# Kernel tuning notes

Hardware: AMD Instinct MI355X
Metric: run time of the kernel (lower is better)

The kernel has to match this reference:

```python
import jax, jax.numpy as jnp
import numpy as np

N_NODES, NUM_FEAT, EMB, HID, N_CLASSES, N_EDGES = 800, 111, 32, 200, 15, 8000
ALPHA = 0.5   # DirGNNConv default mixing
EPS = 1e-5    # LayerNorm eps


def _pade_coeffs(deg=5):
    # [5/5] Pade approximant of sqrt(1 - x) (as in FastDifferentiableMatSqrt)
    K = 2 * deg + 1
    b = np.zeros(K); b[0] = 1.0
    for k in range(1, K):
        b[k] = b[k - 1] * (0.5 - (k - 1)) / k
    c = b * ((-1.0) ** np.arange(K))  # Taylor coeffs of sqrt(1-x)
    A = np.empty((deg, deg))
    for i in range(deg):
        for j in range(1, deg + 1):
            A[i, j - 1] = c[deg + 1 + i - j]
    q = np.concatenate([[1.0], np.linalg.solve(A, -c[deg + 1:])])
    p = np.array([sum(q[j] * c[k - j] for j in range(min(k, deg) + 1)) for k in range(deg + 1)])
    return p.astype(np.float32), q.astype(np.float32)

PADE_P, PADE_Q = _pade_coeffs()


def _mpa_impl(A):
    # matrix square root via Pade approximant (MPA forward)
    normA = jnp.sqrt(jnp.sum(A * A))
    I = jnp.eye(A.shape[0], dtype=A.dtype)
    p_app = I - A / normA
    p_hat = p_app
    p_sqrt = PADE_P[0] * I
    q_sqrt = PADE_Q[0] * I
    for i in range(5):
        p_sqrt = p_sqrt + PADE_P[i + 1] * p_hat
        q_sqrt = q_sqrt + PADE_Q[i + 1] * p_hat
        p_hat = p_hat @ p_app
    return jnp.linalg.solve(q_sqrt, p_sqrt) * jnp.sqrt(normA)


@jax.custom_vjp
def mpa_lya(A):
    return _mpa_impl(A)


def _mpa_fwd(A):
    S = _mpa_impl(A)
    return S, (S, jnp.sqrt(jnp.sum(A * A)))


def _mpa_bwd(res, g):
    # iterative Lyapunov solver backward (8 coupled Newton-Schulz iterations)
    S, normA = res
    I = jnp.eye(S.shape[0], dtype=S.dtype)
    b = S / jnp.sqrt(normA)
    c = g / jnp.sqrt(normA)
    for _ in range(8):
        b2 = b @ b
        c = 0.5 * (c @ (3.0 * I - b2) - b2 @ c + b @ (c @ b))
        b = 0.5 * (b @ (3.0 * I - b2))
    return (0.5 * c,)

mpa_lya.defvjp(_mpa_fwd, _mpa_bwd)


def gcn_sparse(m, ei, n):
    # GCNConv(normalize=False): out[dst] = sum_{(src,dst) in E} (x @ W)[src]
    return jax.ops.segment_sum(m[ei[0]], ei[1], num_segments=n)


def hetero_layer_sparse(h, eis, W, b):
    # W: [3(in,out,root), 4 edge types, Fin, Fout]; HeteroConv aggr='sum'
    n = h.shape[0]
    out = jnp.zeros((n, W.shape[-1]), h.dtype)
    for e, ei in enumerate(eis):
        x_in = gcn_sparse(h @ W[0, e], ei, n) + b[0, e]
        x_out = gcn_sparse(h @ W[1, e], ei[::-1], n) + b[1, e]  # flipped edges
        out = out + ALPHA * x_out + (1.0 - ALPHA) * x_in + h @ W[2, e] + b[2, e]
    return out


def hetero_layer_dense(h, masks, W, b):
    # masks: [4, N, N] binary adjacency (src, dst); dense equivalent of scatter
    out = jnp.zeros((h.shape[0], W.shape[-1]), h.dtype)
    for e in range(masks.shape[0]):
        x_in = masks[e].T @ (h @ W[0, e]) + b[0, e]
        x_out = masks[e] @ (h @ W[1, e]) + b[1, e]
        out = out + ALPHA * x_out + (1.0 - ALPHA) * x_in + h @ W[2, e] + b[2, e]
    return out


def graph_layernorm(h, wb):
    # PyG LayerNorm mode='graph', single graph: normalize over all nodes+feats
    mu = jnp.mean(h)
    var = jnp.mean((h - mu) ** 2)
    return (h - mu) / jnp.sqrt(var + EPS) * wb[0] + wb[1]


def hetero_gnn(h, layer_fn, graph, W1, b1, W2, b2, ln):
    h = graph_layernorm(layer_fn(h, graph, W1, b1), ln[0])
    return graph_layernorm(layer_fn(h, graph, W2, b2), ln[1])


def pairwise_S(z, lin_W, lin_b, iu, ju):
    n = z.shape[0]
    M = (z[iu] - z[ju]) ** 2                        # [N(N+1)/2, HID]
    mg = jax.nn.sigmoid(M @ lin_W + lin_b)[:, 0]    # upper-tri entries, row-major
    tri = jnp.zeros((n, n), z.dtype).at[iu, ju].set(mg)
    return mpa_lya(tri)


def model_forward(x_note, embed_W, embed_b, g1_l1_W, g1_l1_b, g1_l2_W, g1_l2_b, g1_ln,
                  g2_l1_W, g2_l1_b, g2_l2_W, g2_l2_b, g2_ln, lin_W, lin_b, clf_W, clf_b,
                  eis, batch):
    n = x_note.shape[0]
    iu, ju = np.triu_indices(n)
    h = x_note @ embed_W + embed_b                   # [N, 32]
    z0 = hetero_gnn(h, hetero_layer_sparse, eis, g1_l1_W, g1_l1_b, g1_l2_W, g1_l2_b, g1_ln)
    S1 = pairwise_S(z0, lin_W, lin_b, iu, ju)
    A0 = jnp.stack([jnp.zeros((n, n), h.dtype).at[ei[0], ei[1]].set(1.0) for ei in eis])
    h = S1 @ h
    # adj_to_coord(nonzero) only keeps the binary pattern of S1 @ A @ S1
    mask1 = jnp.stack([((S1 @ A0[e]) @ S1 != 0).astype(h.dtype) for e in range(4)])
    z1 = hetero_gnn(h, hetero_layer_dense, mask1, g2_l1_W, g2_l1_b, g2_l2_W, g2_l2_b, g2_ln)
    S2 = pairwise_S(z1, lin_W, lin_b, iu, ju)
    h = S2 @ h
    mask2 = jnp.stack([((S2 @ mask1[e]) @ S2 != 0).astype(h.dtype) for e in range(4)])
    z2 = hetero_gnn(h, hetero_layer_dense, mask2, g2_l1_W, g2_l1_b, g2_l2_W, g2_l2_b, g2_ln)
    counts = jax.ops.segment_sum(jnp.ones((n,), z2.dtype), batch, num_segments=1)
    x2 = jax.ops.segment_sum(z2, batch, num_segments=1) / counts[:, None]  # global_mean_pool
    logits = x2 @ clf_W + clf_b
    return x2, jax.nn.log_softmax(logits, axis=-1), S1, S2


def setup_inputs() -> dict:
    key = jax.random.key(0)
    ks = jax.random.split(key, 14)
    N, F, E, H, NC, NE = N_NODES, NUM_FEAT, EMB, HID, N_CLASSES, N_EDGES
    def w(k, shape, fan_in):
        return (jax.random.normal(k, shape, jnp.float32) / np.sqrt(fan_in)).astype(jnp.float32)
    ln = jnp.broadcast_to(jnp.stack([jnp.ones(H, jnp.float32), jnp.zeros(H, jnp.float32)]), (2, 2, H)) + 0.0
    return dict(
        x_note=jax.random.normal(ks[0], (N, F), jnp.float32),
        embed_W=w(ks[1], (F, E), F), embed_b=jnp.zeros((E,), jnp.float32),
        g1_l1_W=w(ks[2], (3, 4, E, H), E), g1_l1_b=jnp.zeros((3, 4, H), jnp.float32),
        g1_l2_W=w(ks[3], (3, 4, H, H), H), g1_l2_b=jnp.zeros((3, 4, H), jnp.float32),
        g1_ln=ln,
        g2_l1_W=w(ks[4], (3, 4, E, H), E), g2_l1_b=jnp.zeros((3, 4, H), jnp.float32),
        g2_l2_W=w(ks[5], (3, 4, H, H), H), g2_l2_b=jnp.zeros((3, 4, H), jnp.float32),
        g2_ln=ln,
        lin_W=w(ks[6], (H, 1), H), lin_b=jnp.zeros((1,), jnp.float32),
        clf_W=w(ks[7], (H, NC), H), clf_b=jnp.zeros((NC,), jnp.float32),
        ei_forward=jax.random.randint(ks[8], (2, NE), 0, N, jnp.int32),
        ei_onset=jax.random.randint(ks[9], (2, NE), 0, N, jnp.int32),
        ei_sustain=jax.random.randint(ks[10], (2, NE), 0, N, jnp.int32),
        ei_rest=jax.random.randint(ks[11], (2, NE), 0, N, jnp.int32),
        batch=jnp.zeros((N,), jnp.int32),
    )


def reference(x_note, embed_W, embed_b, g1_l1_W, g1_l1_b, g1_l2_W, g1_l2_b, g1_ln,
              g2_l1_W, g2_l1_b, g2_l2_W, g2_l2_b, g2_ln, lin_W, lin_b, clf_W, clf_b,
              ei_forward, ei_onset, ei_sustain, ei_rest, batch):
    eis = (ei_forward, ei_onset, ei_sustain, ei_rest)
    return model_forward(x_note, embed_W, embed_b, g1_l1_W, g1_l1_b, g1_l2_W, g1_l2_b, g1_ln,
                         g2_l1_W, g2_l1_b, g2_l2_W, g2_l2_b, g2_ln, lin_W, lin_b, clf_W, clf_b,
                         eis, batch)
```

## Files before the change

### kernel.cpp

```cpp
#include <hip/hip_runtime.h>
#include <hip/hip_bf16.h>
#include <math.h>
#include <stdio.h>

static constexpr int   kN  = 800;
static constexpr int   kF  = 111;
static constexpr int   kE  = 32;
static constexpr int   kH  = 200;
static constexpr int   kNC = 15;
static constexpr int   kNE = 8000;
static constexpr long  kNN = (long)kN*kN;
static constexpr long  kNH = (long)kN*kH;
static constexpr float kAl  = 0.5f;
static constexpr float kEps = 1e-5f;
static constexpr int   kGB  = (int)((kNH+255)/256);
static constexpr int   kDB  = 50;
static constexpr int   kCH  = 50;
static constexpr int   kNCHK= kN/kCH;

typedef unsigned short u16;
typedef __attribute__((ext_vector_type(8))) short short8;
typedef __attribute__((ext_vector_type(4))) float f32x4;

__device__ __forceinline__ u16 f2bf(float v){
  __hip_bfloat16 b = __float2bfloat16(v);
  return *reinterpret_cast<u16*>(&b);
}
__device__ __forceinline__ float bf2f(u16 h){
  unsigned int u = ((unsigned int)h) << 16;
  float f; __builtin_memcpy(&f, &u, 4);
  return f;
}

enum { EPI_NONE=0, EPI_BIAS=1, EPI_SCALE=4, EPI_ACC=6, EPI_DUAL=7 };

template<bool TRANSA, bool TRIUA, bool TRIUB, int EPI, bool LNA>
__global__ __launch_bounds__(256)
void gemm_kernel(const float* __restrict__ A, int lda,
                 const float* __restrict__ B, int ldb,
                 float* __restrict__ C, int ldc,
                 int M, int Ncl, int K,
                 long sA, long sB, long sC, float scale,
                 const float* __restrict__ bias, int kstep,
                 const double* __restrict__ scalp,
                 const float* __restrict__ lnw,
                 const double* __restrict__ lnpart, int lnnb,
                 float* __restrict__ C2)
{
  constexpr int TM=64, TN=64, TK=16;
  A += (long)blockIdx.z * sA;
  B += (long)blockIdx.z * sB;
  C += (long)blockIdx.z * sC;
  __shared__ float As[TK][TM+4];
  __shared__ float Bs[TK][TN+4];
  const int tid = threadIdx.x;
  const int tn4 = (tid & 15)*4, tm4 = (tid >> 4)*4;
  const int m0 = blockIdx.x * TM, n0 = blockIdx.y * TN;
  float acc[4][4] = {};
  float mu = 0.f, rsf = 1.f;
  if (LNA){
    __shared__ double lnS[256], lnQ[256];
    double s=0.0, q=0.0;
    for (int i=tid; i<lnnb; i+=256){ s += lnpart[2*i]; q += lnpart[2*i+1]; }
    lnS[tid]=s; lnQ[tid]=q;
    __syncthreads();
    for (int h=128; h>0; h>>=1){
      if (tid < h){ lnS[tid]+=lnS[tid+h]; lnQ[tid]+=lnQ[tid+h]; }
      __syncthreads();
    }
    double m = lnS[0]/(double)kNH;
    double var = lnQ[0]/(double)kNH - m*m;
    mu = (float)m;
    rsf = rsqrtf((float)var + kEps);
    __syncthreads();
  }
  const int kbase = kstep ? (int)blockIdx.z * kstep : 0;
  int k0 = TRIUA ? max(m0 - kbase, 0) : 0;
  int kEnd = TRIUB ? min(K, n0 + TN - kbase) : K;
  const bool skip = (k0 >= kEnd);
  if (skip && EPI == EPI_ACC) return;
  if (!skip) {
    float ar[4], br[4];
    auto loadT = [&](int kk0, float* arr, float* brr){
      #pragma unroll
      for (int u=0; u<4; ++u){
        int idx = tid + 256*u;
        float av = 0.f;
        if (!TRANSA) {
          int m = idx >> 4, ka = idx & 15;
          int gm = m0+m, gk = kk0+ka;
          if (gm < M && gk < K){
            av = A[(long)gm*lda + gk];
            if (LNA) av = (av - mu)*(rsf*lnw[gk]) + lnw[kH + gk];
          }
        } else {
          int ka = idx >> 6, m = idx & 63;
          int gm = m0+m, gk = kk0+ka;
          if (gm < M && gk < K){
            av = A[(long)gk*lda + gm];
            if (LNA) av = (av - mu)*(rsf*lnw[gk]) + lnw[kH + gk];
          }
        }
        int kb = idx >> 6, nb = idx & 63;
        int gk = kk0+kb, gn = n0+nb;
        arr[u] = av;
        brr[u] = (gk < K && gn < Ncl) ? B[(long)gk*ldb + gn] : 0.f;
      }
    };
    auto storeT = [&](const float* arr, const float* brr){
      #pragma unroll
      for (int u=0; u<4; ++u){
        int idx = tid + 256*u;
        if (!TRANSA){ int m = idx>>4, ka = idx&15; As[ka][m] = arr[u]; }
        else        { int ka = idx>>6, m = idx&63; As[ka][m] = arr[u]; }
        int kb = idx>>6, nb = idx&63;
        Bs[kb][nb] = brr[u];
      }
    };
    loadT(k0, ar, br);
    for (;;){
      __syncthreads();
      storeT(ar, br);
      __syncthreads();
      int kn = k0 + TK;
      bool more = kn < kEnd;
      if (more) loadT(kn, ar, br);
      #pragma unroll
      for (int kk=0; kk<TK; ++kk) {
        float a[4], b[4];
        #pragma unroll
        for (int u=0;u<4;++u){ a[u]=As[kk][tm4+u]; b[u]=Bs[kk][tn4+u]; }
        #pragma unroll
        for (int i=0;i<4;++i)
          #pragma unroll
          for (int j=0;j<4;++j)
            acc[i][j] = fmaf(a[i], b[j], acc[i][j]);
      }
      if (!more) break;
      k0 = kn;
    }
  }
  float sc = scale;
  if ((EPI == EPI_ACC || EPI == EPI_SCALE || EPI == EPI_DUAL) && scalp)
    sc *= (float)sqrt(sqrt(scalp[0]));
  #pragma unroll
  for (int i=0;i<4;++i) {
    int gm = m0 + tm4 + i;
    if (gm >= M) continue;
    #pragma unroll
    for (int j=0;j<4;++j) {
      int gn = n0 + tn4 + j;
      if (gn >= Ncl) continue;
      float v = acc[i][j];
      long off = (long)gm*ldc + gn;
      if (EPI == EPI_BIAS)       C[off] = v + bias[gn];
      else if (EPI == EPI_SCALE) C[off] = sc*v;
      else if (EPI == EPI_ACC)   unsafeAtomicAdd(&C[off], sc*v);
      else if (EPI == EPI_DUAL){ C[off] = v; C2[off] = sc*v; }
      else                       C[off] = v;
    }
  }
}

template<bool TRANSA, bool TRIUA, bool TRIUB, int EPI, bool LNA = false>
static inline void launch_gemm(hipStream_t st,
                               const float* A, int lda, const float* B, int ldb,
                               float* C, int ldc, int M, int Ncl, int K, int batch,
                               long sA, long sB, long sC, float scale,
                               const float* bias = nullptr, int kstep = 0,
                               const double* scalp = nullptr,
                               const float* lnw = nullptr,
                               const double* lnpart = nullptr, int lnnb = 0,
                               float* C2 = nullptr)
{
  dim3 grid((M+63)/64, (Ncl+63)/64, batch);
  gemm_kernel<TRANSA,TRIUA,TRIUB,EPI,LNA><<<grid, 256, 0, st>>>(
      A,lda,B,ldb,C,ldc,M,Ncl,K,sA,sB,sC,scale,bias,kstep,scalp,lnw,lnpart,lnnb,C2);
}

__global__ __launch_bounds__(256)
void bgemm2_kernel(const u16* __restrict__ Ah, const u16* __restrict__ Al,
                   const u16* __restrict__ Bh, const u16* __restrict__ Bl,
                   float* __restrict__ C, float* __restrict__ C2,
                   u16* __restrict__ Oh, u16* __restrict__ Ol,
                   float p0, float p1)
{
  constexpr int TM=64, TN=64, BK=32;
  __shared__ u16 Ash[TM][40], Asl[TM][40], Bsh[TN][40], Bsl[TN][40];
  const int tid = threadIdx.x;
  const int m0 = blockIdx.x*TM, n0 = blockIdx.y*TN;
  const int w = tid>>6, lane = tid&63;
  const int wm = (w&1)*32, wn = (w>>1)*32;
  const int quad = lane>>4, lm = lane&15;
  f32x4 acc00={}, acc01={}, acc10={}, acc11={};
  const bool skip = (m0 > n0 + TN - 1);
  int k0 = m0;
  const int kEnd = min(kN, n0+TN);
  const int ar = tid>>2, ac = (tid&3)*8;
  if (!skip){
    uint4 avh, avl, bvh, bvl;
    auto loadT = [&](int kk0){
      avh = {0,0,0,0}; avl = {0,0,0,0}; bvh = {0,0,0,0}; bvl = {0,0,0,0};
      int gk = kk0 + ac;
      if (m0+ar < kN && gk < kN){
        avh = *(const uint4*)(Ah + (long)(m0+ar)*kN + gk);
        avl = *(const uint4*)(Al + (long)(m0+ar)*kN + gk);
      }
      if (n0+ar < kN && gk < kN){
        bvh = *(const uint4*)(Bh + (long)(n0+ar)*kN + gk);
        bvl = *(const uint4*)(Bl + (long)(n0+ar)*kN + gk);
      }
    };
    loadT(k0);
    for (;;){
      __syncthreads();
      *(uint4*)&Ash[ar][ac] = avh; *(uint4*)&Asl[ar][ac] = avl;
      *(uint4*)&Bsh[ar][ac] = bvh; *(uint4*)&Bsl[ar][ac] = bvl;
      __syncthreads();
      int kn = k0 + BK;
      bool more = kn < kEnd;
      if (more) loadT(kn);
      short8 a0h = *(const short8*)&Ash[wm+lm][quad*8];
      short8 a1h = *(const short8*)&Ash[wm+16+lm][quad*8];
      short8 a0l = *(const short8*)&Asl[wm+lm][quad*8];
      short8 a1l = *(const short8*)&Asl[wm+16+lm][quad*8];
      short8 b0h = *(const short8*)&Bsh[wn+lm][quad*8];
      short8 b1h = *(const short8*)&Bsh[wn+16+lm][quad*8];
      short8 b0l = *(const short8*)&Bsl[wn+lm][quad*8];
      short8 b1l = *(const short8*)&Bsl[wn+16+lm][quad*8];
      acc00 = __builtin_amdgcn_mfma_f32_16x16x32_bf16(a0h,b0h,acc00,0,0,0);
      acc00 = __builtin_amdgcn_mfma_f32_16x16x32_bf16(a0h,b0l,acc00,0,0,0);
      acc00 = __builtin_amdgcn_mfma_f32_16x16x32_bf16(a0l,b0h,acc00,0,0,0);
      acc01 = __builtin_amdgcn_mfma_f32_16x16x32_bf16(a0h,b1h,acc01,0,0,0);
      acc01 = __builtin_amdgcn_mfma_f32_16x16x32_bf16(a0h,b1l,acc01,0,0,0);
      acc01 = __builtin_amdgcn_mfma_f32_16x16x32_bf16(a0l,b1h,acc01,0,0,0);
      acc10 = __builtin_amdgcn_mfma_f32_16x16x32_bf16(a1h,b0h,acc10,0,0,0);
      acc10 = __builtin_amdgcn_mfma_f32_16x16x32_bf16(a1h,b0l,acc10,0,0,0);
      acc10 = __builtin_amdgcn_mfma_f32_16x16x32_bf16(a1l,b0h,acc10,0,0,0);
      acc11 = __builtin_amdgcn_mfma_f32_16x16x32_bf16(a1h,b1h,acc11,0,0,0);
      acc11 = __builtin_amdgcn_mfma_f32_16x16x32_bf16(a1h,b1l,acc11,0,0,0);
      acc11 = __builtin_amdgcn_mfma_f32_16x16x32_bf16(a1l,b1h,acc11,0,0,0);
      if (!more) break;
      k0 = kn;
    }
  }
  f32x4 accs[2][2] = {{acc00, acc01},{acc10, acc11}};
  #pragma unroll
  for (int ti=0; ti<2; ++ti){
    #pragma unroll
    for (int tj=0; tj<2; ++tj){
      #pragma unroll
      for (int r=0; r<4; ++r){
        int gm = m0 + wm + ti*16 + quad*4 + r;
        int gn = n0 + wn + tj*16 + lm;
        if (gm >= kN || gn >= kN) continue;
        float v = accs[ti][tj][r];
        long off = (long)gm*kN + gn;
        C[off]  += p0*v;
        C2[off] += p1*v;
        if (Oh){
          u16 h = f2bf(v);
          Oh[off] = h;
          Ol[off] = f2bf(v - bf2f(h));
        }
      }
    }
  }
}

__global__ __launch_bounds__(256)
void ln_pair_prep_kernel(const float* __restrict__ tnh, const double* __restrict__ part,
                         int nb, const float* __restrict__ ln, const float* __restrict__ linW,
                         u16* __restrict__ zwh, u16* __restrict__ zwl,
                         u16* __restrict__ zzh, u16* __restrict__ zzl,
                         float* __restrict__ avec, double* __restrict__ frobz)
{
  __shared__ double ss[256], qq[256];
  __shared__ float ared[256];
  const int n = blockIdx.x, t = threadIdx.x;
  if (t == 0) *frobz = 0.0;
  double s=0.0, q=0.0;
  for (int i=t; i<nb; i+=256){ s += part[2*i]; q += part[2*i+1]; }
  ss[t]=s; qq[t]=q;
  __syncthreads();
  for (int h=128; h>0; h>>=1){
    if (t < h){ ss[t]+=ss[t+h]; qq[t]+=qq[t+h]; }
    __syncthreads();
  }
  double m = ss[0]/(double)kNH;
  const float mu = (float)m;
  const float rs = rsqrtf((float)(qq[0]/(double)kNH - m*m) + kEps);
  float acc = 0.f;
  if (t < kH){
    float z = (tnh[(long)n*kH + t] - mu)*(rs*ln[t]) + ln[kH + t];
    float wv = linW[t];
    float zw = wv*z;
    long off = (long)n*kH + t;
    u16 h1 = f2bf(zw);
    zwh[off] = h1; zwl[off] = f2bf(zw - bf2f(h1));
    u16 h2 = f2bf(z);
    zzh[off] = h2; zzl[off] = f2bf(z - bf2f(h2));
    acc = zw*z;
  }
  ared[t] = acc;
  __syncthreads();
  for (int h=128; h>0; h>>=1){
    if (t < h) ared[t] += ared[t+h];
    __syncthreads();
  }
  if (t == 0) avec[n] = ared[0];
}

__global__ __launch_bounds__(256)
void bgemm_pair_kernel(const u16* __restrict__ Ah, const u16* __restrict__ Al,
                       const u16* __restrict__ Bh, const u16* __restrict__ Bl,
                       const float* __restrict__ avec, const float* __restrict__ linb,
                       float* __restrict__ tri, double* __restrict__ frob2)
{
  constexpr int TM=64, TN=64, BK=32, KK=kH;
  __shared__ u16 Ash[TM][40], Asl[TM][40], Bsh[TN][40], Bsl[TN][40];
  __shared__ float red[256];
  const int tid = threadIdx.x;
  const int m0 = blockIdx.x*TM, n0 = blockIdx.y*TN;
  if (m0 > n0 + TN - 1){
    for (int idx = tid; idx < TM*TN; idx += 256){
      int r = idx >> 6, c = idx & 63;
      int gm = m0 + r, gn = n0 + c;
      if (gm < kN && gn < kN) tri[(long)gm*kN + gn] = 0.f;
    }
    return;
  }
  const int w = tid>>6, lane = tid&63;
  const int wm = (w&1)*32, wn = (w>>1)*32;
  const int quad = lane>>4, lm = lane&15;
  f32x4 acc00={}, acc01={}, acc10={}, acc11={};
  const int ar = tid>>2, ac = (tid&3)*8;
  for (int k0 = 0; k0 < KK; k0 += BK){
    uint4 avh={0,0,0,0}, avl={0,0,0,0}, bvh={0,0,0,0}, bvl={0,0,0,0};
    int gk = k0 + ac;
    if (m0+ar < kN && gk < KK){
      avh = *(const uint4*)(Ah + (long)(m0+ar)*KK + gk);
      avl = *(const uint4*)(Al + (long)(m0+ar)*KK + gk);
    }
    if (n0+ar < kN && gk < KK){
      bvh = *(const uint4*)(Bh + (long)(n0+ar)*KK + gk);
      bvl = *(const uint4*)(Bl + (long)(n0+ar)*KK + gk);
    }
    __syncthreads();
    *(uint4*)&Ash[ar][ac] = avh; *(uint4*)&Asl[ar][ac] = avl;
    *(uint4*)&Bsh[ar][ac] = bvh; *(uint4*)&Bsl[ar][ac] = bvl;
    __syncthreads();
    short8 a0h = *(const short8*)&Ash[wm+lm][quad*8];
    short8 a1h = *(const short8*)&Ash[wm+16+lm][quad*8];
    short8 a0l = *(const short8*)&Asl[wm+lm][quad*8];
    short8 a1l = *(const short8*)&Asl[wm+16+lm][quad*8];
    short8 b0h = *(const short8*)&Bsh[wn+lm][quad*8];
    short8 b1h = *(const short8*)&Bsh[wn+16+lm][quad*8];
    short8 b0l = *(const short8*)&Bsl[wn+lm][quad*8];
    short8 b1l = *(const short8*)&Bsl[wn+16+lm][quad*8];
    acc00 = __builtin_amdgcn_mfma_f32_16x16x32_bf16(a0h,b0h,acc00,0,0,0);
    acc00 = __builtin_amdgcn_mfma_f32_16x16x32_bf16(a0h,b0l,acc00,0,0,0);
    acc00 = __builtin_amdgcn_mfma_f32_16x16x32_bf16(a0l,b0h,acc00,0,0,0);
    acc01 = __builtin_amdgcn_mfma_f32_16x16x32_bf16(a0h,b1h,acc01,0,0,0);
    acc01 = __builtin_amdgcn_mfma_f32_16x16x32_bf16(a0h,b1l,acc01,0,0,0);
    acc01 = __builtin_amdgcn_mfma_f32_16x16x32_bf16(a0l,b1h,acc01,0,0,0);
    acc10 = __builtin_amdgcn_mfma_f32_16x16x32_bf16(a1h,b0h,acc10,0,0,0);
    acc10 = __builtin_amdgcn_mfma_f32_16x16x32_bf16(a1h,b0l,acc10,0,0,0);
    acc10 = __builtin_amdgcn_mfma_f32_16x16x32_bf16(a1l,b0h,acc10,0,0,0);
    acc11 = __builtin_amdgcn_mfma_f32_16x16x32_bf16(a1h,b1h,acc11,0,0,0);
    acc11 = __builtin_amdgcn_mfma_f32_16x16x32_bf16(a1h,b1l,acc11,0,0,0);
    acc11 = __builtin_amdgcn_mfma_f32_16x16x32_bf16(a1l,b1h,acc11,0,0,0);
  }
  const float lb = linb[0];
  float r2 = 0.f;
  f32x4 accs[2][2] = {{acc00, acc01},{acc10, acc11}};
  #pragma unroll
  for (int ti=0; ti<2; ++ti){
    #pragma unroll
    for (int tj=0; tj<2; ++tj){
      #pragma unroll
      for (int r=0; r<4; ++r){
        int gm = m0 + wm + ti*16 + quad*4 + r;
        int gn = n0 + wn + tj*16 + lm;
        if (gm >= kN || gn >= kN) continue;
        float t = 0.f;
        if (gm <= gn){
          float marg = avec[gm] + avec[gn] - 2.f*accs[ti][tj][r] + lb;
          t = 1.f/(1.f + expf(-marg));
        }
        tri[(long)gm*kN + gn] = t;
        r2 += t*t;
      }
    }
  }
  red[tid] = r2;
  __syncthreads();
  for (int h=128; h>0; h>>=1){
    if (tid < h) red[tid] += red[tid+h];
    __syncthreads();
  }
  if (tid == 0) unsafeAtomicAdd(frob2, (double)red[0]);
}

__global__ __launch_bounds__(256)
void pade_both_kernel(const float* __restrict__ tri, const double* __restrict__ frob2,
                      u16* __restrict__ ph, u16* __restrict__ pl,
                      u16* __restrict__ th, u16* __restrict__ tl,
                      float* __restrict__ psq, float* __restrict__ qsq,
                      float P0, float P1, float Q0, float Q1)
{
  __shared__ float t[32][33];
  const float rn = (float)(1.0 / sqrt(frob2[0]));
  int r0 = blockIdx.y*32, c0 = blockIdx.x*32;
  int tr = threadIdx.x>>5, tc = threadIdx.x&31;
  for (int i=tr; i<32; i+=8){
    int r = r0+i, c = c0+tc;
    float eye = (r==c) ? 1.f : 0.f;
    float pa = eye - tri[(long)r*kN + c]*rn;
    t[i][tc] = pa;
    long off = (long)r*kN + c;
    psq[off] = P0*eye + P1*pa;
    qsq[off] = Q0*eye + Q1*pa;
    u16 h = f2bf(pa);
    ph[off] = h;
    pl[off] = f2bf(pa - bf2f(h));
  }
  __syncthreads();
  for (int i=tr; i<32; i+=8){
    int c = c0+i, r = r0+tc;
    float v = t[tc][i];
    u16 h = f2bf(v);
    th[(long)c*kN + r] = h;
    tl[(long)c*kN + r] = f2bf(v - bf2f(h));
  }
}

__device__ __forceinline__ float bias_comb(const float* __restrict__ b, int i){
  float v = 0.f;
  #pragma unroll
  for (int e=0;e<4;++e)
    v += (1.f-kAl)*b[(0*4+e)*kH + i] + kAl*b[(1*4+e)*kH + i] + b[(2*4+e)*kH + i];
  return v;
}

__global__ __launch_bounds__(256)
void prep_kernel(const float* __restrict__ g1w1, const float* __restrict__ g1b1,
                 const float* __restrict__ g1w2, const float* __restrict__ g1b2,
                 const float* __restrict__ g2w1, const float* __restrict__ g2b1,
                 const float* __restrict__ g2w2, const float* __restrict__ g2b2,
                 float* __restrict__ wc1, float* __restrict__ wc2,
                 float* __restrict__ wc3, float* __restrict__ wc4,
                 float* __restrict__ bs, int* __restrict__ cnt, int* __restrict__ g)
{
  constexpr int EH = kE*kH, HH = kH*kH;
  long i = (long)blockIdx.x*256 + threadIdx.x;
  if (i < 8L*EH){ wc1[i] = g1w1[i]; return; } i -= 8L*EH;
  if (i < EH){
    float v=0.f;
    #pragma unroll
    for (int e=0;e<4;++e) v += g1w1[(long)(8+e)*EH + i];
    wc1[8L*EH+i] = v; return;
  } i -= EH;
  if (i < 8L*HH){ wc2[i] = g1w2[i]; return; } i -= 8L*HH;
  if (i < HH){
    float v=0.f;
    #pragma unroll
    for (int e=0;e<4;++e) v += g1w2[(long)(8+e)*HH + i];
    wc2[8L*HH+i] = v; return;
  } i -= HH;
  if (i < 8L*EH){ wc3[i] = g2w1[i]; return; } i -= 8L*EH;
  if (i < EH){
    float v=0.f;
    #pragma unroll
    for (int e=0;e<4;++e) v += g2w1[(long)(8+e)*EH + i];
    wc3[8L*EH+i] = v; return;
  } i -= EH;
  if (i < 8L*HH){ wc4[i] = g2w2[i]; return; } i -= 8L*HH;
  if (i < HH){
    float v=0.f;
    #pragma unroll
    for (int e=0;e<4;++e) v += g2w2[(long)(8+e)*HH + i];
    wc4[8L*HH+i] = v; return;
  } i -= HH;
  if (i < kH){ bs[i]        = bias_comb(g1b1, (int)i); return; } i -= kH;
  if (i < kH){ bs[kH+i]     = bias_comb(g1b2, (int)i); return; } i -= kH;
  if (i < kH){ bs[2*kH+i]   = bias_comb(g2b1, (int)i); return; } i -= kH;
  if (i < kH){ bs[3*kH+i]   = bias_comb(g2b2, (int)i); return; } i -= kH;
  if (i < 8L*kN){ cnt[i] = 0; return; } i -= 8L*kN;
  if (i < 4L*kN){ g[i] = -1; return; }
}

__global__ void edge_cg_kernel(const int* __restrict__ e0, const int* __restrict__ e1,
                               const int* __restrict__ e2, const int* __restrict__ e3,
                               int* __restrict__ cnt, int* __restrict__ g){
  const int* eis[4] = {e0,e1,e2,e3};
  const int e = blockIdx.y;
  const int* ei = eis[e];
  int j = blockIdx.x*256 + threadIdx.x;
  if (j >= kNE) return;
  int s = ei[j], d = ei[kNE + j];
  atomicAdd(&cnt[e*kN + d], 1);
  atomicAdd(&cnt[(4+e)*kN + s], 1);
  atomicMax(&g[e*kN + d], s);
}

__global__ __launch_bounds__(256)
void scan12_kernel(const int* __restrict__ cnt, int* __restrict__ offs, int* __restrict__ cur,
                   int* __restrict__ g, int* __restrict__ h){
  __shared__ int buf[kN+1];
  const int b = blockIdx.x, t = threadIdx.x;
  if (b < 8){
    for (int i=t; i<kN; i+=256) buf[i] = cnt[b*kN + i];
    __syncthreads();
    if (t == 0){
      int acc = 0;
      for (int i=0;i<kN;++i){ int c = buf[i]; buf[i] = acc; acc += c; }
      buf[kN] = acc;
    }
    __syncthreads();
    for (int i=t; i<kN; i+=256){ offs[b*(kN+1)+i] = buf[i]; cur[b*kN+i] = buf[i]; }
    if (t == 0) offs[b*(kN+1)+kN] = buf[kN];
  } else {
    const int e = b - 8;
    for (int i=t; i<kN; i+=256) buf[i] = g[e*kN + i];
    __syncthreads();
    if (t == 0){
      int m = -1;
      for (int i=0;i<kN;++i){ m = max(m, buf[i]); buf[i] = m; }
    }
    __syncthreads();
    for (int i=t; i<kN; i+=256) g[e*kN + i] = buf[i];
    for (int d=t; d<kN; d+=256){
      int lo = 0, hi = kN;
      while (lo < hi){ int mid = (lo+hi)>>1; if (buf[mid] >= d) hi = mid; else lo = mid+1; }
      h[e*kN + d] = lo;
    }
  }
}

__global__ void edge_fill_kernel(const int* __restrict__ e0, const int* __restrict__ e1,
                                 const int* __restrict__ e2, const int* __restrict__ e3,
                                 int* __restrict__ cur, int* __restrict__ adj){
  const int* eis[4] = {e0,e1,e2,e3};
  const int e = blockIdx.y;
  const int* ei = eis[e];
  int j = blockIdx.x*256 + threadIdx.x;
  if (j >= kNE) return;
  int s = ei[j], d = ei[kNE + j];
  int p = atomicAdd(&cur[e*kN + d], 1);
  adj[(long)e*kNE + p] = s;
  int q = atomicAdd(&cur[(4+e)*kN + s], 1);
  adj[(long)(4+e)*kNE + q] = d;
}

__global__ __launch_bounds__(256)
void gather_sparse_kernel(const float* __restrict__ Y, const int* __restrict__ offs,
                          const int* __restrict__ adj, const float* __restrict__ bsum,
                          float* __restrict__ tnh, double* __restrict__ part){
  __shared__ double ss[256], qq[256];
  const int n = blockIdx.x;
  const int f = threadIdx.x;
  double sp = 0.0, qp = 0.0;
  float acc = 0.f;
  if (f < kH){
    #pragma unroll
    for (int l = 0; l < 8; ++l){
      const float* Yp = Y + (long)l*kNH;
      int b = offs[l*(kN+1) + n], e2 = offs[l*(kN+1) + n + 1];
      for (int idx = b; idx < e2; ++idx){
        int m = adj[(long)l*kNE + idx];
        acc += Yp[(long)m*kH + f];
      }
    }
    float t = Y[(long)8*kNH + (long)n*kH + f] + bsum[f] + 0.5f*acc;
    tnh[(long)n*kH + f] = t;
    sp = t; qp = (double)t*t;
  }
  ss[threadIdx.x]=sp; qq[threadIdx.x]=qp;
  __syncthreads();
  for (int hh=128; hh>0; hh>>=1){
    if ((int)threadIdx.x < hh){ ss[threadIdx.x]+=ss[threadIdx.x+hh]; qq[threadIdx.x]+=qq[threadIdx.x+hh]; }
    __syncthreads();
  }
  if (threadIdx.x==0){ part[2*blockIdx.x]=ss[0]; part[2*blockIdx.x+1]=qq[0]; }
}

__global__ __launch_bounds__(256)
void scan_chunk_kernel(float* __restrict__ Y, float* __restrict__ Tot){
  const int plane = blockIdx.y;
  const int chunk = blockIdx.x;
  const int f = threadIdx.x;
  if (f >= kH) return;
  float* P = Y + (long)plane*kNH + (long)chunk*kCH*kH + f;
  float acc = 0.f;
  if (plane < 4){
    for (int i0 = 0; i0 < kCH; i0 += 5){
      float v0 = P[(long)(i0+0)*kH], v1 = P[(long)(i0+1)*kH], v2 = P[(long)(i0+2)*kH],
            v3 = P[(long)(i0+3)*kH], v4 = P[(long)(i0+4)*kH];
      acc += v0; P[(long)(i0+0)*kH] = acc;
      acc += v1; P[(long)(i0+1)*kH] = acc;
      acc += v2; P[(long)(i0+2)*kH] = acc;
      acc += v3; P[(long)(i0+3)*kH] = acc;
      acc += v4; P[(long)(i0+4)*kH] = acc;
    }
  } else {
    for (int i0 = kCH-1; i0 >= 4; i0 -= 5){
      float v0 = P[(long)(i0-0)*kH], v1 = P[(long)(i0-1)*kH], v2 = P[(long)(i0-2)*kH],
            v3 = P[(long)(i0-3)*kH], v4 = P[(long)(i0-4)*kH];
      acc += v0; P[(long)(i0-0)*kH] = acc;
      acc += v1; P[(long)(i0-1)*kH] = acc;
      acc += v2; P[(long)(i0-2)*kH] = acc;
      acc += v3; P[(long)(i0-3)*kH] = acc;
      acc += v4; P[(long)(i0-4)*kH] = acc;
    }
  }
  Tot[((long)plane*kNCHK + chunk)*kH + f] = acc;
}

__global__ __launch_bounds__(256)
void gather_dense_kernel(const float* __restrict__ Y, const int* __restrict__ g,
                         const int* __restrict__ h, const float* __restrict__ bsum,
                         const float* __restrict__ Tot,
                         float* __restrict__ tnh, double* __restrict__ part){
  __shared__ double ss[256], qq[256];
  long idx = (long)blockIdx.x*256 + threadIdx.x;
  double s = 0.0, q = 0.0;
  if (idx < kNH){
    int n = (int)(idx / kH), f = (int)(idx % kH);
    float v = 0.f;
    #pragma unroll
    for (int e = 0; e < 4; ++e){
      int gi = g[e*kN + n];
      if (gi >= 0){
        v += Y[(long)e*kNH + (long)gi*kH + f];
        int cg = (int)((unsigned)gi / (unsigned)kCH);
        const float* T = Tot + (long)e*kNCHK*kH + f;
        for (int cc = 0; cc < cg; ++cc) v += T[(long)cc*kH];
      }
      int hi = h[e*kN + n];
      if (hi < kN){
        v += Y[(long)(4+e)*kNH + (long)hi*kH + f];
        int ch = (int)((unsigned)hi / (unsigned)kCH);
        const float* T = Tot + (long)(4+e)*kNCHK*kH + f;
        for (int cc = ch+1; cc < kNCHK; ++cc) v += T[(long)cc*kH];
      }
    }
    float t = Y[(long)8*kNH + idx] + bsum[f] + 0.5f*v;
    tnh[idx] = t;
    s = t; q = (double)t*t;
  }
  ss[threadIdx.x]=s; qq[threadIdx.x]=q;
  __syncthreads();
  for (int hh=128; hh>0; hh>>=1){
    if ((int)threadIdx.x < hh){ ss[threadIdx.x]+=ss[threadIdx.x+hh]; qq[threadIdx.x]+=qq[threadIdx.x+hh]; }
    __syncthreads();
  }
  if (threadIdx.x==0){ part[2*blockIdx.x]=ss[0]; part[2*blockIdx.x+1]=qq[0]; }
}

__global__ __launch_bounds__(64)
void invdiag_kernel(const float* __restrict__ U, float* __restrict__ W){
  __shared__ float Us[kDB][kDB+1];
  __shared__ float Xs[kDB][kDB+1];
  const int base = blockIdx.x * kDB;
  const int tid = threadIdx.x;
  for (int idx = tid; idx < kDB*kDB; idx += 64){
    int r = idx / kDB, c = idx % kDB;
    Us[r][c] = U[(long)(base+r)*kN + base + c];
  }
  __syncthreads();
  const int c = tid;
  for (int i = kDB-1; i >= 0; --i){
    if (c < kDB){
      float x;
      if (c < i) x = 0.f;
      else {
        float s = 0.f;
        for (int k = i+1; k < kDB; ++k) s = fmaf(Us[i][k], Xs[k][c], s);
        x = (((c==i)?1.f:0.f) - s) / Us[i][i];
      }
      Xs[i][c] = x;
    }
    __syncthreads();
  }
  for (int idx = tid; idx < kDB*kDB; idx += 64){
    int r = idx / kDB, cc = idx % kDB;
    W[(long)(base+r)*kN + base + cc] = Xs[r][cc];
  }
}

template<int S>
__global__ __launch_bounds__(256)
void merge_fused_kernel(const float* __restrict__ U, float* __restrict__ W){
  __shared__ float Us[S][S+1];
  __shared__ float Wb[S][S+1];
  __shared__ float T[S][S+1];
  const long base = (long)blockIdx.x * (2*S) * (kN+1);
  const int tid = threadIdx.x;
  for (int idx = tid; idx < S*S; idx += 256){
    int r = idx / S, c = idx % S;
    Us[r][c] = U[base + (long)r*kN + S + c];
    Wb[r][c] = W[base + (long)(S+r)*kN + S + c];
  }
  __syncthreads();
  for (int idx = tid; idx < S*S; idx += 256){
    int r = idx / S, c = idx % S;
    float s = 0.f;
    for (int k = 0; k <= c; ++k) s = fmaf(Us[r][k], Wb[k][c], s);
    T[r][c] = s;
  }
  __syncthreads();
  for (int idx = tid; idx < S*S; idx += 256){
    int r = idx / S, c = idx % S;
    Us[r][c] = W[base + (long)r*kN + c];
  }
  __syncthreads();
  for (int idx = tid; idx < S*S; idx += 256){
    int r = idx / S, c = idx % S;
    float s = 0.f;
    for (int k = r; k < S; ++k) s = fmaf(Us[r][k], T[k][c], s);
    W[base + (long)r*kN + S + c] = -s;
  }
}

__global__ __launch_bounds__(256)
void colsum_kernel(const float* __restrict__ tnh, float* __restrict__ colpart){
  const int b = blockIdx.x;
  const int f = threadIdx.x;
  if (f >= kH) return;
  const float* P = tnh + (long)b*16*kH + f;
  float acc = 0.f;
  #pragma unroll
  for (int i = 0; i < 16; ++i) acc += P[(long)i*kH];
  colpart[(long)b*kH + f] = acc;
}

__global__ __launch_bounds__(256)
void pool_head_kernel(const float* __restrict__ colpart, const double* __restrict__ part, int nb,
                      const float* __restrict__ ln,
                      const float* __restrict__ W, const float* __restrict__ b,
                      float* __restrict__ out){
  __shared__ double sred[256], qred[256];
  __shared__ float x2[kH];
  __shared__ float lg[kNC];
  int t = threadIdx.x;
  double s=0.0, q=0.0;
  for (int i=t; i<nb; i+=256){ s += part[2*i]; q += part[2*i+1]; }
  sred[t]=s; qred[t]=q;
  __syncthreads();
  for (int hh=128; hh>0; hh>>=1){
    if (t < hh){ sred[t]+=sred[t+hh]; qred[t]+=qred[t+hh]; }
    __syncthreads();
  }
  const float mu = (float)(sred[0] / (double)kNH);
  const float rs = rsqrtf((float)(qred[0]/(double)kNH - (sred[0]/(double)kNH)*(sred[0]/(double)kNH)) + kEps);
  if (t < kH){
    float sum = 0.f;
    for (int bb = 0; bb < 50; ++bb) sum += colpart[(long)bb*kH + t];
    float v = (sum * (1.f/(float)kN) - mu)*(rs*ln[t]) + ln[kH+t];
    x2[t] = v;
    out[t] = v;
  }
  __syncthreads();
  if (t < kNC){
    float sv = b[t];
    for (int f = 0; f < kH; ++f) sv = fmaf(x2[f], W[f*kNC + t], sv);
    lg[t] = sv;
  }
  __syncthreads();
  if (t == 0){
    float m = -1e30f;
    for (int c=0;c<kNC;++c) m = fmaxf(m, lg[c]);
    float se = 0.f;
    for (int c=0;c<kNC;++c) se += expf(lg[c]-m);
    float lse = m + logf(se);
    for (int c=0;c<kNC;++c) out[kH + c] = lg[c]-lse;
  }
}

static void pade_coeffs(float* P, float* Q){
  double b[11]; b[0] = 1.0;
  for (int k=1;k<11;++k) b[k] = b[k-1]*(0.5-(k-1))/k;
  double c[11];
  for (int k=0;k<11;++k) c[k] = b[k]*((k&1)?-1.0:1.0);
  double A[5][5], rhs[5];
  for (int i=0;i<5;++i){ for (int j=0;j<5;++j) A[i][j] = c[5+i-j]; rhs[i] = -c[6+i]; }
  for (int col=0; col<5; ++col){
    int p = col;
    for (int r=col+1;r<5;++r) if (fabs(A[r][col]) > fabs(A[p][col])) p = r;
    if (p != col){
      for (int j=0;j<5;++j){ double t=A[col][j]; A[col][j]=A[p][j]; A[p][j]=t; }
      double t=rhs[col]; rhs[col]=rhs[p]; rhs[p]=t;
    }
    for (int r=col+1;r<5;++r){
      double f = A[r][col]/A[col][col];
      for (int j=col;j<5;++j) A[r][j] -= f*A[col][j];
      rhs[r] -= f*rhs[col];
    }
  }
  double q[6]; q[0] = 1.0;
  for (int r=4;r>=0;--r){
    double s = rhs[r];
    for (int j=r+1;j<5;++j) s -= A[r][j]*q[1+j];
    q[1+r] = s/A[r][r];
  }
  double p[6];
  for (int k=0;k<6;++k){
    double s = 0.0; int jm = k<5?k:5;
    for (int j=0;j<=jm;++j) s += q[j]*c[k-j];
    p[k] = s;
  }
  for (int k=0;k<6;++k){ P[k]=(float)p[k]; Q[k]=(float)q[k]; }
}

extern "C" void kernel_launch(void* const* d_in, const int* in_sizes, int n_in,
                              void* d_out, int out_size, void* d_ws, size_t ws_size,
                              hipStream_t stream)
{
  const float* x_note = (const float*)d_in[0];
  const float* embW   = (const float*)d_in[1];
  const float* embB   = (const float*)d_in[2];
  const float* g1w1   = (const float*)d_in[3];
  const float* g1b1   = (const float*)d_in[4];
  const float* g1w2   = (const float*)d_in[5];
  const float* g1b2   = (const float*)d_in[6];
  const float* g1ln   = (const float*)d_in[7];
  const float* g2w1   = (const float*)d_in[8];
  const float* g2b1   = (const float*)d_in[9];
  const float* g2w2   = (const float*)d_in[10];
  const float* g2b2   = (const float*)d_in[11];
  const float* g2ln   = (const float*)d_in[12];
  const float* linW   = (const float*)d_in[13];
  const float* linb   = (const float*)d_in[14];
  const float* clfW   = (const float*)d_in[15];
  const float* clfb   = (const float*)d_in[16];
  const int*  e0     = (const int*)d_in[17];
  const int*  e1     = (const int*)d_in[18];
  const int*  e2     = (const int*)d_in[19];
  const int*  e3     = (const int*)d_in[20];
  float* out = (float*)d_out;

  constexpr long o_h0   = 4096;
  constexpr long o_h1   = o_h0   + (long)kN*kE;
  constexpr long o_h2   = o_h1   + (long)kN*kE;
  constexpr long o_tnh  = o_h2   + (long)kN*kE;
  constexpr long o_pp   = o_tnh  + kNH;
  constexpr long o_av   = o_pp   + 2*kNH;
  constexpr long o_big  = o_av   + kN;
  constexpr long o_tri  = o_big  + 4*kNN;
  constexpr long o_sacc = o_tri  + kNN;
  constexpr long o_winv = o_sacc + kNN;
  constexpr long o_psq  = o_winv + kNN;
  constexpr long o_qsq  = o_psq  + kNN;
  constexpr long o_g    = o_qsq  + kNN;
  constexpr long o_hh   = o_g    + 4*kN;
  constexpr long o_wc1  = o_hh   + 4*kN;
  constexpr long o_wc2  = o_wc1  + 9L*kE*kH;
  constexpr long o_wc3  = o_wc2  + 9L*kH*kH;
  constexpr long o_wc4  = o_wc3  + 9L*kE*kH;
  constexpr long o_bs   = o_wc4  + 9L*kH*kH;
  constexpr long o_cnt  = o_bs   + 4*kH;
  constexpr long o_offs = o_cnt  + 8*kN;
  constexpr long o_cur  = o_offs + 8*(kN+1);
  constexpr long o_adj  = o_cur  + 8*kN;
  constexpr long o_end  = o_adj  + 8*(long)kNE;

  if (ws_size < (size_t)o_end*sizeof(float) || out_size < 215 + 2*(int)kNN || n_in < 21){
    fprintf(stderr, "kernel_launch guard: ws=%zu need=%zu out=%d need=%d n_in=%d\n",
            ws_size, (size_t)o_end*sizeof(float), out_size, (int)(215+2*kNN), n_in);
    hipMemsetAsync(d_out, 0, (size_t)out_size*sizeof(float), stream);
    return;
  }

  float* ws = (float*)d_ws;
  double* scald = (double*)d_ws;
  double* partd = (double*)((char*)d_ws + 512);
  float *h0=ws+o_h0, *h1=ws+o_h1, *h2=ws+o_h2, *tnh=ws+o_tnh,
        *big=ws+o_big, *tri=ws+o_tri, *Sacc=ws+o_sacc, *winv=ws+o_winv,
        *psq=ws+o_psq, *qsq=ws+o_qsq;
  u16* zwh = (u16*)(ws + o_pp);
  u16* zwl = zwh + kNH;
  u16* zzh = zwl + kNH;
  u16* zzl = zzh + kNH;
  float* avec = ws + o_av;
  int* gArr = (int*)(ws + o_g);
  int* hArr = (int*)(ws + o_hh);
  float *wc1=ws+o_wc1, *wc2=ws+o_wc2, *wc3=ws+o_wc3, *wc4=ws+o_wc4, *bs=ws+o_bs;
  int* cntA = (int*)(ws + o_cnt);
  int* offsA= (int*)(ws + o_offs);
  int* curA = (int*)(ws + o_cur);
  int* adjA = (int*)(ws + o_adj);
  u16* papp_h = (u16*)big;
  u16* papp_l = papp_h + kNN;
  u16* pT_h   = papp_l + kNN;
  u16* pT_l   = pT_h + kNN;
  u16* pwA_h  = pT_l + kNN;
  u16* pwA_l  = pwA_h + kNN;
  u16* pwB_h  = pwA_l + kNN;
  u16* pwB_l  = pwB_h + kNN;
  float* totbuf  = big + (long)9*kNH;
  float* colpart = totbuf + (long)8*kNCHK*kH;

  float P[6], Q[6];
  pade_coeffs(P, Q);

  auto eg = [](long n){ return dim3((unsigned)((n+255)/256)); };

  auto layer_gemm = [&](const float* hin, int K, const float* wcat,
                        const float* lnp, int nb){
    if (lnp)
      launch_gemm<false,false,false,EPI_NONE,true>(stream, hin, K, wcat, kH, big, kH,
          kN, kH, K, 9, 0, (long)K*kH, kNH, 0.f, nullptr, 0, nullptr, lnp, partd, nb);
    else
      launch_gemm<false,false,false,EPI_NONE>(stream, hin, K, wcat, kH, big, kH,
          kN, kH, K, 9, 0, (long)K*kH, kNH, 0.f);
  };
  auto sparse_layer = [&](const float* hin, int K, const float* wcat, const float* bsum,
                          const float* lnp, int nb){
    layer_gemm(hin, K, wcat, lnp, nb);
    gather_sparse_kernel<<<dim3(kN),256,0,stream>>>(big, offsA, adjA, bsum, tnh, partd);
  };
  auto dense_layer = [&](const float* hin, int K, const float* wcat, const float* bsum,
                         const float* lnp, int nb){
    layer_gemm(hin, K, wcat, lnp, nb);
    scan_chunk_kernel<<<dim3(kNCHK,8),256,0,stream>>>(big, totbuf);
    gather_dense_kernel<<<kGB,256,0,stream>>>(big, gArr, hArr, bsum, totbuf, tnh, partd);
  };
  auto blocked_trsm = [&](float* SoutDst){
    invdiag_kernel<<<dim3(kN/kDB),64,0,stream>>>(qsq, winv);
    merge_fused_kernel<50><<<dim3(kN/100),256,0,stream>>>(qsq, winv);
    {
      int s = 100, npairs = 4;
      long step = (long)2*s*kN + 2*s;
      launch_gemm<false,false,true,EPI_NONE>(stream,
          qsq + s, kN, winv + (long)s*kN + s, kN, tri, s,
          s, s, s, npairs, step, step, (long)s*s, 0.f);
      launch_gemm<false,true,false,EPI_SCALE>(stream,
          winv, kN, tri, s, winv + s, kN,
          s, s, s, npairs, step, (long)s*s, step, -1.f);
    }
    {
      int s = 200, npairs = 2;
      long step = (long)2*s*kN + 2*s;
      launch_gemm<false,false,true,EPI_NONE>(stream,
          qsq + s, kN, winv + (long)s*kN + s, kN, tri, s,
          s, s, s, npairs, step, step, (long)s*s, 0.f);
      launch_gemm<false,true,false,EPI_SCALE>(stream,
          winv, kN, tri, s, winv + s, kN,
          s, s, s, npairs, step, (long)s*s, step, -1.f);
    }
    {
      launch_gemm<false,false,true,EPI_NONE>(stream,
          qsq + 400, kN, winv + (long)400*kN + 400, kN, tri, 400,
          400, 400, 400, 1, 0, 0, 0, 0.f);
      launch_gemm<false,true,false,EPI_SCALE>(stream,
          winv, kN, tri, 400, winv + 400, kN,
          400, 400, 400, 1, 0, 0, 0, -1.f);
    }
    launch_gemm<false,true,true,EPI_DUAL>(stream,
        winv, kN, psq, kN, Sacc, kN, kN, kN, kN, 1,
        0, 0, 0, 1.f, nullptr, 0, scald+3, nullptr, nullptr, 0, SoutDst);
  };
  auto run_pair_mpa = [&](int nb, const float* lnp, float* SoutDst){
    ln_pair_prep_kernel<<<dim3(kN),256,0,stream>>>(tnh, partd, nb, lnp, linW,
                                                   zwh, zwl, zzh, zzl, avec, scald+3);
    bgemm_pair_kernel<<<dim3(13,13),256,0,stream>>>(zwh, zwl, zzh, zzl, avec, linb,
                                                    tri, scald+3);
    pade_both_kernel<<<dim3(25,25),256,0,stream>>>(tri, scald+3, papp_h, papp_l, pT_h, pT_l,
                                                   psq, qsq, P[0],P[1],Q[0],Q[1]);
    dim3 g13(13,13,1);
    bgemm2_kernel<<<g13,256,0,stream>>>(papp_h,papp_l, pT_h,pT_l, psq,qsq, pwA_h,pwA_l, P[2],Q[2]);
    bgemm2_kernel<<<g13,256,0,stream>>>(pwA_h,pwA_l,  pT_h,pT_l, psq,qsq, pwB_h,pwB_l, P[3],Q[3]);
    bgemm2_kernel<<<g13,256,0,stream>>>(pwB_h,pwB_l,  pT_h,pT_l, psq,qsq, pwA_h,pwA_l, P[4],Q[4]);
    bgemm2_kernel<<<g13,256,0,stream>>>(pwA_h,pwA_l,  pT_h,pT_l, psq,qsq, nullptr,nullptr, P[5],Q[5]);
    blocked_trsm(SoutDst);
  };
  auto s_times_h = [&](const float* hin, float* hout){
    launch_gemm<false,true,false,EPI_SCALE>(stream,
        Sacc, kN, hin, kE, hout, kE, kN, kE, kN, 1,
        0, 0, 0, 1.f, nullptr, 0, scald+3);
  };

  float* S1f = out + 215;
  float* S2f = out + 215 + kNN;

  hipMemsetAsync(winv, 0, (size_t)kNN*sizeof(float), stream);
  {
    constexpr long prep_span = 2L*(9L*kE*kH + 9L*kH*kH) + 4L*kH + 8L*kN + 4L*kN;
    prep_kernel<<<eg(prep_span),256,0,stream>>>(g1w1, g1b1, g1w2, g1b2,
                                                g2w1, g2b1, g2w2, g2b2,
                                                wc1, wc2, wc3, wc4, bs, cntA, gArr);
  }
  edge_cg_kernel<<<dim3((kNE+255)/256,4),256,0,stream>>>(e0,e1,e2,e3, cntA, gArr);
  scan12_kernel<<<dim3(12),256,0,stream>>>(cntA, offsA, curA, gArr, hArr);
  edge_fill_kernel<<<dim3((kNE+255)/256,4),256,0,stream>>>(e0,e1,e2,e3, curA, adjA);

  launch_gemm<false,false,false,EPI_BIAS>(stream, x_note, kF, embW, kE, h0, kE, kN, kE, kF, 1,
                                          0,0,0, 0.f, embB);

  sparse_layer(h0,  kE, wc1, bs,      nullptr, 0);
  sparse_layer(tnh, kH, wc2, bs+kH,   g1ln, kN);

  run_pair_mpa(kN, g1ln + 2*kH, S1f);

  s_times_h(h0, h1);

  dense_layer(h1,  kE, wc3, bs+2*kH, nullptr, 0);
  dense_layer(tnh, kH, wc4, bs+3*kH, g2ln, kGB);

  run_pair_mpa(kGB, g2ln + 2*kH, S2f);

  s_times_h(h1, h2);

  dense_layer(h2,  kE, wc3, bs+2*kH, nullptr, 0);
  dense_layer(tnh, kH, wc4, bs+3*kH, g2ln, kGB);

  colsum_kernel<<<dim3(50),256,0,stream>>>(tnh, colpart);
  pool_head_kernel<<<dim3(1),256,0,stream>>>(colpart, partd, kGB, g2ln + 2*kH, clfW, clfb, out);
}
```

Measured before the change: 1.151 ms.

## Split-K the large triangular GEMMs with atomic accumulation and separate scaling pass

The 400x400 trsm update GEMMs, the final 800x800 W^-1·P GEMM, and the S·h GEMM now split K into chunks of 100 across the batch dimension and accumulate into zeroed outputs with atomic adds. This gives these low-occupancy, long-K launches more blocks. The dual-output epilogue is removed and replaced by a separate elementwise kernel that scales Sacc into the output. The cost is extra memsets, atomic traffic, an additional pass over the 800x800 matrix, and a winv memset that now runs on every call.

```diff
diff --git a/kernel.cpp b/kernel.cpp
--- a/kernel.cpp
+++ b/kernel.cpp
@@ -32,7 +32,7 @@
   return f;
 }
 
-enum { EPI_NONE=0, EPI_BIAS=1, EPI_SCALE=4, EPI_ACC=6, EPI_DUAL=7 };
+enum { EPI_NONE=0, EPI_BIAS=1, EPI_SCALE=4, EPI_ACC=6 };
 
 template<bool TRANSA, bool TRIUA, bool TRIUB, int EPI, bool LNA>
 __global__ __launch_bounds__(256)
@@ -44,8 +44,7 @@
                  const float* __restrict__ bias, int kstep,
                  const double* __restrict__ scalp,
                  const float* __restrict__ lnw,
-                 const double* __restrict__ lnpart, int lnnb,
-                 float* __restrict__ C2)
+                 const double* __restrict__ lnpart, int lnnb)
 {
   constexpr int TM=64, TN=64, TK=16;
   A += (long)blockIdx.z * sA;
@@ -141,8 +140,7 @@
     }
   }
   float sc = scale;
-  if ((EPI == EPI_ACC || EPI == EPI_SCALE || EPI == EPI_DUAL) && scalp)
-    sc *= (float)sqrt(sqrt(scalp[0]));
+  if (EPI == EPI_ACC && scalp) sc *= (float)sqrt(sqrt(scalp[0]));
   #pragma unroll
   for (int i=0;i<4;++i) {
     int gm = m0 + tm4 + i;
@@ -154,9 +152,8 @@
       float v = acc[i][j];
       long off = (long)gm*ldc + gn;
       if (EPI == EPI_BIAS)       C[off] = v + bias[gn];
-      else if (EPI == EPI_SCALE) C[off] = sc*v;
+      else if (EPI == EPI_SCALE) C[off] = scale*v;
       else if (EPI == EPI_ACC)   unsafeAtomicAdd(&C[off], sc*v);
-      else if (EPI == EPI_DUAL){ C[off] = v; C2[off] = sc*v; }
       else                       C[off] = v;
     }
   }
@@ -170,12 +167,11 @@
                                const float* bias = nullptr, int kstep = 0,
                                const double* scalp = nullptr,
                                const float* lnw = nullptr,
-                               const double* lnpart = nullptr, int lnnb = 0,
-                               float* C2 = nullptr)
+                               const double* lnpart = nullptr, int lnnb = 0)
 {
   dim3 grid((M+63)/64, (Ncl+63)/64, batch);
   gemm_kernel<TRANSA,TRIUA,TRIUB,EPI,LNA><<<grid, 256, 0, st>>>(
-      A,lda,B,ldb,C,ldc,M,Ncl,K,sA,sB,sC,scale,bias,kstep,scalp,lnw,lnpart,lnnb,C2);
+      A,lda,B,ldb,C,ldc,M,Ncl,K,sA,sB,sC,scale,bias,kstep,scalp,lnw,lnpart,lnnb);
 }
 
 __global__ __launch_bounds__(256)
@@ -435,6 +431,15 @@
   }
 }
 
+__global__ __launch_bounds__(256)
+void copy_scale_kernel(const float* __restrict__ src, const double* __restrict__ frob2,
+                       float* __restrict__ dst)
+{
+  const float fac = (float)sqrt(sqrt(frob2[0]));
+  long i = (long)blockIdx.x*256 + threadIdx.x;
+  if (i < kNN) __builtin_nontemporal_store(src[i]*fac, &dst[i]);
+}
+
 __device__ __forceinline__ float bias_comb(const float* __restrict__ b, int i){
   float v = 0.f;
   #pragma unroll
@@ -926,7 +931,8 @@
     scan_chunk_kernel<<<dim3(kNCHK,8),256,0,stream>>>(big, totbuf);
     gather_dense_kernel<<<kGB,256,0,stream>>>(big, gArr, hArr, bsum, totbuf, tnh, partd);
   };
-  auto blocked_trsm = [&](float* SoutDst){
+  auto blocked_trsm = [&](){
+    hipMemsetAsync(winv, 0, (size_t)kNN*sizeof(float), stream);
     invdiag_kernel<<<dim3(kN/kDB),64,0,stream>>>(qsq, winv);
     merge_fused_kernel<50><<<dim3(kN/100),256,0,stream>>>(qsq, winv);
     {
@@ -950,16 +956,18 @@
           s, s, s, npairs, step, (long)s*s, step, -1.f);
     }
     {
-      launch_gemm<false,false,true,EPI_NONE>(stream,
+      hipMemsetAsync(tri, 0, (size_t)400*400*sizeof(float), stream);
+      launch_gemm<false,false,true,EPI_ACC>(stream,
           qsq + 400, kN, winv + (long)400*kN + 400, kN, tri, 400,
-          400, 400, 400, 1, 0, 0, 0, 0.f);
-      launch_gemm<false,true,false,EPI_SCALE>(stream,
+          400, 400, 100, 4, 100, (long)100*kN, 0, 1.f, nullptr, 100);
+      launch_gemm<false,true,false,EPI_ACC>(stream,
           winv, kN, tri, 400, winv + 400, kN,
-          400, 400, 400, 1, 0, 0, 0, -1.f);
-    }
-    launch_gemm<false,true,true,EPI_DUAL>(stream,
-        winv, kN, psq, kN, Sacc, kN, kN, kN, kN, 1,
-        0, 0, 0, 1.f, nullptr, 0, scald+3, nullptr, nullptr, 0, SoutDst);
+          400, 400, 100, 4, 100, (long)100*400, 0, -1.f, nullptr, 100);
+    }
+    hipMemsetAsync(Sacc, 0, (size_t)kNN*sizeof(float), stream);
+    launch_gemm<false,true,true,EPI_ACC>(stream,
+        winv, kN, psq, kN, Sacc, kN, kN, kN, 100, 8,
+        100, (long)100*kN, 0, 1.f, nullptr, 100);
   };
   auto run_pair_mpa = [&](int nb, const float* lnp, float* SoutDst){
     ln_pair_prep_kernel<<<dim3(kN),256,0,stream>>>(tnh, partd, nb, lnp, linW,
@@ -973,18 +981,19 @@
     bgemm2_kernel<<<g13,256,0,stream>>>(pwA_h,pwA_l,  pT_h,pT_l, psq,qsq, pwB_h,pwB_l, P[3],Q[3]);
     bgemm2_kernel<<<g13,256,0,stream>>>(pwB_h,pwB_l,  pT_h,pT_l, psq,qsq, pwA_h,pwA_l, P[4],Q[4]);
     bgemm2_kernel<<<g13,256,0,stream>>>(pwA_h,pwA_l,  pT_h,pT_l, psq,qsq, nullptr,nullptr, P[5],Q[5]);
-    blocked_trsm(SoutDst);
+    blocked_trsm();
+    copy_scale_kernel<<<eg(kNN),256,0,stream>>>(Sacc, scald+3, SoutDst);
   };
   auto s_times_h = [&](const float* hin, float* hout){
-    launch_gemm<false,true,false,EPI_SCALE>(stream,
-        Sacc, kN, hin, kE, hout, kE, kN, kE, kN, 1,
-        0, 0, 0, 1.f, nullptr, 0, scald+3);
+    hipMemsetAsync(hout, 0, (size_t)kN*kE*sizeof(float), stream);
+    launch_gemm<false,true,false,EPI_ACC>(stream,
+        Sacc, kN, hin, kE, hout, kE, kN, kE, 100, 8,
+        100, (long)100*kE, 0, 1.f, nullptr, 100, scald+3);
   };
 
   float* S1f = out + 215;
   float* S2f = out + 215 + kNN;
 
-  hipMemsetAsync(winv, 0, (size_t)kNN*sizeof(float), stream);
   {
     constexpr long prep_span = 2L*(9L*kE*kH + 9L*kH*kH) + 4L*kH + 8L*kN + 4L*kN;
     prep_kernel<<<eg(prep_span),256,0,stream>>>(g1w1, g1b1, g1w2, g1b2,
```

Result: faster. 1.019 ms (-11.5%).
